# Kernel tuning notes

Measured on AMD Instinct MI355X. Metric: run time of the kernel, lower is better.

Reference implementation:

```python
import jax, jax.numpy as jnp
import numpy as np

LAMBDA_S = 1.0   # options['lambda_s']
NITER = 100      # options['iter_ihs']

_HS_FILTER = jnp.array([[1/12, 1/6, 1/12],
                        [1/6,  0.0, 1/6 ],
                        [1/12, 1/6, 1/12]], dtype=jnp.float32)


def _smooth(f):
    # f: [n, h, w] -> 3x3 Horn-Schunck weighted average, zero padding (== torch conv2d padding=1)
    k = _HS_FILTER.reshape(1, 1, 3, 3)  # [out_c, in_c, kh, kw]
    return jax.lax.conv_general_dilated(f[:, None], k, window_strides=(1, 1), padding='SAME')[:, 0]


def setup_inputs() -> dict:
    key = jax.random.key(0)
    k1, k2 = jax.random.split(key)
    n, h, w = 8, 256, 256
    x = jax.random.normal(k1, (n, 3, h, w), dtype=jnp.float32)            # [I_t, I_x, I_y]
    old_estimate = jax.random.normal(k2, (n, 2, h, w), dtype=jnp.float32)  # warm-start (u, v)
    return {"x": x, "old_estimate": old_estimate}


def reference(x, old_estimate):
    # x: [n,3,h,w]; old_estimate: [n,2,h,w]
    I_t, I_x, I_y = x[:, 0], x[:, 1], x[:, 2]
    denom = LAMBDA_S ** 2 + I_x ** 2 + I_y ** 2  # iteration-invariant
    u0, v0 = old_estimate[:, 0], old_estimate[:, 1]  # warm_ihs=True

    def step(carry, _):
        u, v = carry
        u_bar = _smooth(u)
        v_bar = _smooth(v)
        der = (I_x * u_bar + I_y * v_bar + I_t) / denom
        return (u_bar - I_x * der, v_bar - I_y * der), None

    (u, v), _ = jax.lax.scan(step, (u0, v0), None, length=NITER)
    return jnp.stack((u, v), axis=1)  # [n,2,h,w]
```

## Files before the change

### kernel.cpp

```cpp
#include <hip/hip_runtime.h>

typedef unsigned long long ull;

#define HH 256
#define WW 256
#define PLANE (HH*WW)
#define TILE_R 32
#define TILE_C 64
#define TT 8
#define ER (TILE_R + 2*TT)
#define EC (TILE_C + 2*TT)
#define NCP (EC/2)
#define NRG 8
#define RPT (ER/NRG)
#define NTHR 320
#define LSZ (4 + ER*EC*2 + 4)

#define RING_OFS (2u*1024u*1024u)
#define FLAG_OFS (4u*1024u*1024u)
#define RIMG (HH*(WW/2)*4)
#define NBLK 256

__device__ __forceinline__ void hs_step(
    const float* __restrict__ rbuf, float* __restrict__ wbuf,
    int fb, int rm, int r0, int rN,
    float4* __restrict__ Mreg,
    const float2* __restrict__ ca, const float2* __restrict__ cb,
    const float2* __restrict__ cc, const float2* __restrict__ cd,
    const float2* __restrict__ ce)
{
    const float* qb = rbuf + fb;

    float2 L[RPT+2], R[RPT+2];
    const float* p0 = qb + 160*rm;
    const float* pN = qb + 160*rN;
    L[0] = *(const float2*)(p0 - 2);  R[0] = *(const float2*)(p0 + 4);
    #pragma unroll
    for (int j = 0; j < RPT; ++j) {
        const float* pr = qb + 160*(r0 + j);
        L[j+1] = *(const float2*)(pr - 2);
        R[j+1] = *(const float2*)(pr + 4);
    }
    L[RPT+1] = *(const float2*)(pN - 2);  R[RPT+1] = *(const float2*)(pN + 4);
    float4 Mb0 = *(const float4*)(p0);
    float4 MbN = *(const float4*)(pN);

    float2 hu[RPT+2], hv[RPT+2];
    hu[0] = make_float2(fmaf(2.f,Mb0.x,L[0].x)+Mb0.z, fmaf(2.f,Mb0.z,Mb0.x)+R[0].x);
    hv[0] = make_float2(fmaf(2.f,Mb0.y,L[0].y)+Mb0.w, fmaf(2.f,Mb0.w,Mb0.y)+R[0].y);
    #pragma unroll
    for (int j = 0; j < RPT; ++j) {
        float4 Mc = Mreg[j];
        hu[j+1] = make_float2(fmaf(2.f,Mc.x,L[j+1].x)+Mc.z, fmaf(2.f,Mc.z,Mc.x)+R[j+1].x);
        hv[j+1] = make_float2(fmaf(2.f,Mc.y,L[j+1].y)+Mc.w, fmaf(2.f,Mc.w,Mc.y)+R[j+1].y);
    }
    hu[RPT+1] = make_float2(fmaf(2.f,MbN.x,L[RPT+1].x)+MbN.z, fmaf(2.f,MbN.z,MbN.x)+R[RPT+1].x);
    hv[RPT+1] = make_float2(fmaf(2.f,MbN.y,L[RPT+1].y)+MbN.w, fmaf(2.f,MbN.w,MbN.y)+R[RPT+1].y);

    #pragma unroll
    for (int j = 0; j < RPT; ++j) {
        float4 Mc = Mreg[j];
        float tux = fmaf(-4.f, Mc.x, fmaf(2.f, hu[j+1].x, hu[j].x) + hu[j+2].x);
        float tuy = fmaf(-4.f, Mc.z, fmaf(2.f, hu[j+1].y, hu[j].y) + hu[j+2].y);
        float tvx = fmaf(-4.f, Mc.y, fmaf(2.f, hv[j+1].x, hv[j].x) + hv[j+2].x);
        float tvy = fmaf(-4.f, Mc.w, fmaf(2.f, hv[j+1].y, hv[j].y) + hv[j+2].y);
        float2 un, vn;
        un.x = fmaf(ca[j].x, tux, -fmaf(cb[j].x, tvx, cc[j].x));
        un.y = fmaf(ca[j].y, tuy, -fmaf(cb[j].y, tvy, cc[j].y));
        vn.x = fmaf(cd[j].x, tvx, -fmaf(cb[j].x, tux, ce[j].x));
        vn.y = fmaf(cd[j].y, tvy, -fmaf(cb[j].y, tuy, ce[j].y));
        float4 nv = make_float4(un.x, vn.x, un.y, vn.y);
        *(float4*)(wbuf + 160*(r0 + j) + fb) = nv;
        Mreg[j] = nv;
    }
}

__global__ __launch_bounds__(NTHR, 2)
void hs_mega(const float* __restrict__ x,
             const float* __restrict__ est,
             float* __restrict__ out,
             float* __restrict__ ws)
{
    __shared__ __align__(16) float s0[LSZ];
    __shared__ __align__(16) float s1[LSZ];

    const int img = blockIdx.x, cs = blockIdx.y, rb = blockIdx.z;
    const int tid = threadIdx.x;
    const int er0 = rb*TILE_R - TT;
    const int ec0 = cs*TILE_C - TT;
    const int blin = (img*4 + cs)*8 + rb;
    unsigned* flags = (unsigned*)(ws + FLAG_OFS);

    int nb = -1;
    if (tid < 8) {
        int t = (tid < 4) ? tid : tid + 1;
        int dr = t/3 - 1, dc = t%3 - 1;
        int nrb = rb + dr, ncs = cs + dc;
        if (nrb >= 0 && nrb < 8 && ncs >= 0 && ncs < 4)
            nb = (img*4 + ncs)*8 + nrb;
    }

    const int cp = tid % NCP;
    const int rg = tid / NCP;
    const int r0 = rg * RPT;
    const int fb = 4 + 4*cp;
    const int rm = (r0 == 0) ? 0 : r0 - 1;
    const int rN = (r0 + RPT > ER-1) ? ER-1 : r0+RPT;

    float2 ca[RPT], cb[RPT], cc[RPT], cd[RPT], ce[RPT];
    {
        const float* __restrict__ xit = x + img*3*PLANE;
        const float* __restrict__ xix = xit + PLANE;
        const float* __restrict__ xiy = xix + PLANE;
        #pragma unroll
        for (int i = 0; i < RPT; ++i) {
            int gr = er0 + r0 + i;
            #pragma unroll
            for (int j = 0; j < 2; ++j) {
                int gc = ec0 + 2*cp + j;
                float A=0.f, B=0.f, C=0.f, D=0.f, E=0.f;
                if (gr >= 0 && gr < HH && gc >= 0 && gc < WW) {
                    int q = gr*WW + gc;
                    float it = xit[q], ix = xix[q], iy = xiy[q];
                    float rd = 1.0f / (1.0f + ix*ix + iy*iy);
                    const float s12 = 1.0f/12.0f;
                    A = (1.0f - ix*ix*rd) * s12;
                    B = (ix*iy*rd) * s12;
                    C = ix*it*rd;
                    D = (1.0f - iy*iy*rd) * s12;
                    E = iy*it*rd;
                }
                if (j == 0) { ca[i].x=A; cb[i].x=B; cc[i].x=C; cd[i].x=D; ce[i].x=E; }
                else        { ca[i].y=A; cb[i].y=B; cc[i].y=C; cd[i].y=D; ce[i].y=E; }
            }
        }
    }

    {
        const float* __restrict__ eu = est + img*2*PLANE;
        const float* __restrict__ ev = eu + PLANE;
        for (int k = tid; k < ER*NCP; k += NTHR) {
            int r = k / NCP, c = k - r*NCP;
            int gr = er0 + r, gc = ec0 + 2*c;
            float2 uu = make_float2(0.f,0.f), vv = make_float2(0.f,0.f);
            if (gr >= 0 && gr < HH && gc >= 0 && gc < WW) {
                uu = *(const float2*)(eu + gr*WW + gc);
                vv = *(const float2*)(ev + gr*WW + gc);
            }
            *(float4*)(s0 + 4 + 160*r + 4*c) = make_float4(uu.x, vv.x, uu.y, vv.y);
        }
    }
    __syncthreads();

    float4 Mreg[RPT];
    #pragma unroll
    for (int j = 0; j < RPT; ++j)
        Mreg[j] = *(const float4*)(s0 + 160*(r0 + j) + fb);

    for (int p = 0; p < 13; ++p) {
        if (p < 12) {
            #pragma unroll
            for (int q = 0; q < 4; ++q) {
                hs_step(s0, s1, fb, rm, r0, rN, Mreg, ca, cb, cc, cd, ce);
                __syncthreads();
                hs_step(s1, s0, fb, rm, r0, rN, Mreg, ca, cb, cc, cd, ce);
                __syncthreads();
            }
        } else {
            #pragma unroll
            for (int q = 0; q < 2; ++q) {
                hs_step(s0, s1, fb, rm, r0, rN, Mreg, ca, cb, cc, cd, ce);
                __syncthreads();
                hs_step(s1, s0, fb, rm, r0, rN, Mreg, ca, cb, cc, cd, ce);
                __syncthreads();
            }
        }

        if (p < 12) {
            float* ring = ws + (unsigned)(p & 1) * RING_OFS + img*RIMG;

            for (int k = tid; k < 640; k += NTHR) {
                int m = k; int r, c2;
                if (m < 256)      { r = m >> 5;              c2 = m & 31; }
                else if (m < 512) { r = 24 + ((m-256) >> 5); c2 = (m-256) & 31; }
                else { int mm = m - 512; r = 8 + (mm >> 3); int t = mm & 7; c2 = (t < 4) ? t : 24 + t; }
                const float* sp = s0 + 4 + 160*(r + TT) + 4*(c2 + 4);
                float* gp = ring + ((rb*TILE_R + r)*(WW/2) + cs*(TILE_C/2) + c2)*4;
                __hip_atomic_store((ull*)gp,     *(const ull*)sp,       __ATOMIC_RELAXED, __HIP_MEMORY_SCOPE_AGENT);
                __hip_atomic_store((ull*)gp + 1, *(const ull*)(sp + 2), __ATOMIC_RELAXED, __HIP_MEMORY_SCOPE_AGENT);
            }
            asm volatile("s_waitcnt vmcnt(0)" ::: "memory");
            __syncthreads();
            if (tid == 0)
                __hip_atomic_store(&flags[p*NBLK + blin], 0x5eed0100u + (unsigned)p,
                                   __ATOMIC_RELAXED, __HIP_MEMORY_SCOPE_AGENT);
            asm volatile("" ::: "memory");
            if (tid < 8 && nb >= 0) {
                const unsigned tgt = 0x5eed0100u + (unsigned)p;
                while (__hip_atomic_load(&flags[p*NBLK + nb],
                                         __ATOMIC_RELAXED, __HIP_MEMORY_SCOPE_AGENT) != tgt)
                    __builtin_amdgcn_s_sleep(1);
            }
            __syncthreads();

            for (int k = tid; k < 896; k += NTHR) {
                int m = k; int r, c2;
                if (m < 320)      { r = m / 40;              c2 = m - (m/40)*40; }
                else if (m < 640) { int mm = m-320; r = 40 + mm/40; c2 = mm - (mm/40)*40; }
                else { int mm = m - 640; r = 8 + (mm >> 3); int t = mm & 7; c2 = (t < 4) ? t : 32 + t; }
                int gr = er0 + r, gc2 = cs*(TILE_C/2) - 4 + c2;
                ull v0 = 0, v1 = 0;
                if (gr >= 0 && gr < HH && gc2 >= 0 && gc2 < WW/2) {
                    const float* gp = ring + (gr*(WW/2) + gc2)*4;
                    v0 = __hip_atomic_load((const ull*)gp,     __ATOMIC_RELAXED, __HIP_MEMORY_SCOPE_AGENT);
                    v1 = __hip_atomic_load((const ull*)gp + 1, __ATOMIC_RELAXED, __HIP_MEMORY_SCOPE_AGENT);
                }
                float* sp = s0 + 4 + 160*r + 4*c2;
                *(ull*)sp = v0;
                *(ull*)(sp + 2) = v1;
            }
            __syncthreads();

            #pragma unroll
            for (int j = 0; j < RPT; ++j)
                Mreg[j] = *(const float4*)(s0 + 160*(r0 + j) + fb);
        }
    }

    {
        float* ou = out + img*2*PLANE;
        float* ov = ou + PLANE;
        for (int k = tid; k < 1024; k += NTHR) {
            int r = k >> 5, c2 = k & 31;
            float4 V = *(const float4*)(s0 + 4 + 160*(r + TT) + 4*(c2 + 4));
            int q = (rb*TILE_R + r)*WW + cs*TILE_C + 2*c2;
            *(float2*)(ou + q) = make_float2(V.x, V.z);
            *(float2*)(ov + q) = make_float2(V.y, V.w);
        }
    }
}

extern "C" void kernel_launch(void* const* d_in, const int* in_sizes, int n_in,
                              void* d_out, int out_size, void* d_ws, size_t ws_size,
                              hipStream_t stream) {
    const float* x   = (const float*)d_in[0];
    const float* est = (const float*)d_in[1];
    float* out = (float*)d_out;
    float* ws  = (float*)d_ws;

    dim3 grid(8, WW/TILE_C, HH/TILE_R);
    dim3 blk(NTHR);
    hs_mega<<<grid, blk, 0, stream>>>(x, est, out, ws);
}
```

Measured before the change: 193.9 us.

## Widen halo to 16 to halve inter-block boundary exchanges

Doubles the halo depth of each tile from 8 to 16, so each block runs 16 Horn-Schunck iterations locally between global exchanges. That cuts the number of flag-synchronised ring-buffer exchanges from 12 to 6. The cost is more redundant halo computation per step (a larger extended tile), more threads per block, and larger LDS buffers. The buffers move to dynamic shared memory sized above the static limit, which likely allows only one block per CU.

```diff
diff --git a/kernel.cpp b/kernel.cpp
--- a/kernel.cpp
+++ b/kernel.cpp
@@ -7,14 +7,16 @@
 #define PLANE (HH*WW)
 #define TILE_R 32
 #define TILE_C 64
-#define TT 8
+#define TT 16
 #define ER (TILE_R + 2*TT)
 #define EC (TILE_C + 2*TT)
 #define NCP (EC/2)
 #define NRG 8
 #define RPT (ER/NRG)
-#define NTHR 320
-#define LSZ (4 + ER*EC*2 + 4)
+#define NTHR 384
+#define RS 192
+#define LBUF (4 + ER*RS + 4)
+#define SMEM_BYTES (2*LBUF*4)
 
 #define RING_OFS (2u*1024u*1024u)
 #define FLAG_OFS (4u*1024u*1024u)
@@ -32,12 +34,12 @@
     const float* qb = rbuf + fb;
 
     float2 L[RPT+2], R[RPT+2];
-    const float* p0 = qb + 160*rm;
-    const float* pN = qb + 160*rN;
+    const float* p0 = qb + RS*rm;
+    const float* pN = qb + RS*rN;
     L[0] = *(const float2*)(p0 - 2);  R[0] = *(const float2*)(p0 + 4);
     #pragma unroll
     for (int j = 0; j < RPT; ++j) {
-        const float* pr = qb + 160*(r0 + j);
+        const float* pr = qb + RS*(r0 + j);
         L[j+1] = *(const float2*)(pr - 2);
         R[j+1] = *(const float2*)(pr + 4);
     }
@@ -70,7 +72,7 @@
         vn.x = fmaf(cd[j].x, tvx, -fmaf(cb[j].x, tux, ce[j].x));
         vn.y = fmaf(cd[j].y, tvy, -fmaf(cb[j].y, tuy, ce[j].y));
         float4 nv = make_float4(un.x, vn.x, un.y, vn.y);
-        *(float4*)(wbuf + 160*(r0 + j) + fb) = nv;
+        *(float4*)(wbuf + RS*(r0 + j) + fb) = nv;
         Mreg[j] = nv;
     }
 }
@@ -81,8 +83,9 @@
              float* __restrict__ out,
              float* __restrict__ ws)
 {
-    __shared__ __align__(16) float s0[LSZ];
-    __shared__ __align__(16) float s1[LSZ];
+    extern __shared__ __align__(16) float smem[];
+    float* s0 = smem;
+    float* s1 = smem + LBUF;
 
     const int img = blockIdx.x, cs = blockIdx.y, rb = blockIdx.z;
     const int tid = threadIdx.x;
@@ -147,7 +150,7 @@
                 uu = *(const float2*)(eu + gr*WW + gc);
                 vv = *(const float2*)(ev + gr*WW + gc);
             }
-            *(float4*)(s0 + 4 + 160*r + 4*c) = make_float4(uu.x, vv.x, uu.y, vv.y);
+            *(float4*)(s0 + 4 + RS*r + 4*c) = make_float4(uu.x, vv.x, uu.y, vv.y);
         }
     }
     __syncthreads();
@@ -155,36 +158,24 @@
     float4 Mreg[RPT];
     #pragma unroll
     for (int j = 0; j < RPT; ++j)
-        Mreg[j] = *(const float4*)(s0 + 160*(r0 + j) + fb);
-
-    for (int p = 0; p < 13; ++p) {
-        if (p < 12) {
-            #pragma unroll
-            for (int q = 0; q < 4; ++q) {
-                hs_step(s0, s1, fb, rm, r0, rN, Mreg, ca, cb, cc, cd, ce);
-                __syncthreads();
-                hs_step(s1, s0, fb, rm, r0, rN, Mreg, ca, cb, cc, cd, ce);
-                __syncthreads();
-            }
-        } else {
-            #pragma unroll
-            for (int q = 0; q < 2; ++q) {
-                hs_step(s0, s1, fb, rm, r0, rN, Mreg, ca, cb, cc, cd, ce);
-                __syncthreads();
-                hs_step(s1, s0, fb, rm, r0, rN, Mreg, ca, cb, cc, cd, ce);
-                __syncthreads();
-            }
-        }
-
-        if (p < 12) {
+        Mreg[j] = *(const float4*)(s0 + RS*(r0 + j) + fb);
+
+    for (int p = 0; p < 7; ++p) {
+        const int ndbl = (p < 6) ? (TT/2) : 2;
+
+        for (int q = 0; q < ndbl; ++q) {
+            hs_step(s0, s1, fb, rm, r0, rN, Mreg, ca, cb, cc, cd, ce);
+            __syncthreads();
+            hs_step(s1, s0, fb, rm, r0, rN, Mreg, ca, cb, cc, cd, ce);
+            __syncthreads();
+        }
+
+        if (p < 6) {
             float* ring = ws + (unsigned)(p & 1) * RING_OFS + img*RIMG;
 
-            for (int k = tid; k < 640; k += NTHR) {
-                int m = k; int r, c2;
-                if (m < 256)      { r = m >> 5;              c2 = m & 31; }
-                else if (m < 512) { r = 24 + ((m-256) >> 5); c2 = (m-256) & 31; }
-                else { int mm = m - 512; r = 8 + (mm >> 3); int t = mm & 7; c2 = (t < 4) ? t : 24 + t; }
-                const float* sp = s0 + 4 + 160*(r + TT) + 4*(c2 + 4);
+            for (int k = tid; k < TILE_R*(TILE_C/2); k += NTHR) {
+                int r = k >> 5, c2 = k & 31;
+                const float* sp = s0 + 4 + RS*(r + TT) + 4*(c2 + TT/2);
                 float* gp = ring + ((rb*TILE_R + r)*(WW/2) + cs*(TILE_C/2) + c2)*4;
                 __hip_atomic_store((ull*)gp,     *(const ull*)sp,       __ATOMIC_RELAXED, __HIP_MEMORY_SCOPE_AGENT);
                 __hip_atomic_store((ull*)gp + 1, *(const ull*)(sp + 2), __ATOMIC_RELAXED, __HIP_MEMORY_SCOPE_AGENT);
@@ -203,19 +194,19 @@
             }
             __syncthreads();
 
-            for (int k = tid; k < 896; k += NTHR) {
+            for (int k = tid; k < 2048; k += NTHR) {
                 int m = k; int r, c2;
-                if (m < 320)      { r = m / 40;              c2 = m - (m/40)*40; }
-                else if (m < 640) { int mm = m-320; r = 40 + mm/40; c2 = mm - (mm/40)*40; }
-                else { int mm = m - 640; r = 8 + (mm >> 3); int t = mm & 7; c2 = (t < 4) ? t : 32 + t; }
-                int gr = er0 + r, gc2 = cs*(TILE_C/2) - 4 + c2;
+                if (m < 768)       { r = m / NCP;              c2 = m - (m/NCP)*NCP; }
+                else if (m < 1536) { int mm = m-768; r = 48 + mm/NCP; c2 = mm - (mm/NCP)*NCP; }
+                else { int mm = m - 1536; r = 16 + (mm >> 4); int t = mm & 15; c2 = (t < 8) ? t : 32 + t; }
+                int gr = er0 + r, gc2 = cs*(TILE_C/2) - TT/2 + c2;
                 ull v0 = 0, v1 = 0;
                 if (gr >= 0 && gr < HH && gc2 >= 0 && gc2 < WW/2) {
                     const float* gp = ring + (gr*(WW/2) + gc2)*4;
                     v0 = __hip_atomic_load((const ull*)gp,     __ATOMIC_RELAXED, __HIP_MEMORY_SCOPE_AGENT);
                     v1 = __hip_atomic_load((const ull*)gp + 1, __ATOMIC_RELAXED, __HIP_MEMORY_SCOPE_AGENT);
                 }
-                float* sp = s0 + 4 + 160*r + 4*c2;
+                float* sp = s0 + 4 + RS*r + 4*c2;
                 *(ull*)sp = v0;
                 *(ull*)(sp + 2) = v1;
             }
@@ -223,16 +214,16 @@
 
             #pragma unroll
             for (int j = 0; j < RPT; ++j)
-                Mreg[j] = *(const float4*)(s0 + 160*(r0 + j) + fb);
+                Mreg[j] = *(const float4*)(s0 + RS*(r0 + j) + fb);
         }
     }
 
     {
         float* ou = out + img*2*PLANE;
         float* ov = ou + PLANE;
-        for (int k = tid; k < 1024; k += NTHR) {
+        for (int k = tid; k < TILE_R*(TILE_C/2); k += NTHR) {
             int r = k >> 5, c2 = k & 31;
-            float4 V = *(const float4*)(s0 + 4 + 160*(r + TT) + 4*(c2 + 4));
+            float4 V = *(const float4*)(s0 + 4 + RS*(r + TT) + 4*(c2 + TT/2));
             int q = (rb*TILE_R + r)*WW + cs*TILE_C + 2*c2;
             *(float2*)(ou + q) = make_float2(V.x, V.z);
             *(float2*)(ov + q) = make_float2(V.y, V.w);
@@ -248,7 +239,10 @@
     float* out = (float*)d_out;
     float* ws  = (float*)d_ws;
 
+    hipFuncSetAttribute((const void*)hs_mega,
+                        hipFuncAttributeMaxDynamicSharedMemorySize, SMEM_BYTES);
+
     dim3 grid(8, WW/TILE_C, HH/TILE_R);
     dim3 blk(NTHR);
-    hs_mega<<<grid, blk, 0, stream>>>(x, est, out, ws);
+    hs_mega<<<grid, blk, SMEM_BYTES, stream>>>(x, est, out, ws);
 }
```

After: 195.9 us. Within noise of the previous version (+1.0%).
